# Optimization experiments

Measured on AMD Instinct MI355X. Metric: run time of the kernel, lower is better.

## Reference

```python
import jax, jax.numpy as jnp
import numpy as np

NUM_CLASS = 31
B = 4096
F_IN = 2048
F_BOT = 256


def setup_inputs() -> dict:
    key = jax.random.key(0)
    ks = jax.random.split(key, 6)
    return {
        "source": jax.random.normal(ks[0], (B, F_IN), dtype=jnp.float32),
        "target": jax.random.normal(ks[1], (B, F_IN), dtype=jnp.float32),
        "W_b": jax.random.normal(ks[2], (F_IN, F_BOT), dtype=jnp.float32) * (1.0 / np.sqrt(F_IN)),
        "b_b": jnp.zeros((F_BOT,), dtype=jnp.float32),
        "W_c": jax.random.normal(ks[3], (F_BOT, NUM_CLASS), dtype=jnp.float32) * (1.0 / np.sqrt(F_BOT)),
        "b_c": jnp.zeros((NUM_CLASS,), dtype=jnp.float32),
        "source_label": jax.random.randint(ks[4], (B,), 0, NUM_CLASS, dtype=jnp.int64),
    }


def _conf_margin(logits, labels):
    # get_confidence_output_margin: softmax confidence margin vs best wrong class
    conf = jax.nn.softmax(logits, axis=-1)
    mask = jax.nn.one_hot(labels, NUM_CLASS, dtype=conf.dtype)
    targets_conf = jnp.sum(conf * mask, axis=1)
    max_excl_conf = jnp.max(conf * (1.0 - mask), axis=1)
    return targets_conf - max_excl_conf


def _pairwise_sqdist(s, t):
    # ||x_p - x_q||^2 computed as a single GEMM + broadcast (replaces python double loop)
    s2 = jnp.sum(s * s, axis=1)  # [Bs]
    t2 = jnp.sum(t * t, axis=1)  # [Bt]
    d2 = s2[:, None] + t2[None, :] - 2.0 * (s @ t.T)
    return jnp.maximum(d2, 0.0)


def reference(source, target, W_b, b_b, W_c, b_c, source_label):
    # bottleneck: Linear + ReLU (shared weights for both domains)
    src = jax.nn.relu(source @ W_b + b_b)  # [B, 256]
    tar = jax.nn.relu(target @ W_b + b_b)  # [B, 256]

    src_clf = src @ W_c + b_c  # [B, 31]
    tar_clf = tar @ W_c + b_c  # [B, 31]

    # cross entropy on source
    logp = jax.nn.log_softmax(src_clf, axis=-1)
    clf_loss = -jnp.mean(jnp.take_along_axis(logp, source_label[:, None], axis=1))

    src_margin = _conf_margin(src_clf, source_label)
    tar_margin = _conf_margin(tar_clf, jnp.argmax(tar_clf, axis=1))

    # no_grad diagnostics: MMD + Gaussian kernel means (amplitude=1, sigma in {1,5})
    delta = jnp.mean(src, axis=0) - jnp.mean(tar, axis=0)
    curr_mmd = jax.lax.stop_gradient(delta @ delta)
    d2 = _pairwise_sqdist(src, tar)  # [B, B]
    curr_gk1 = jax.lax.stop_gradient(jnp.mean(jnp.exp(-0.5 * d2)))
    curr_gk5 = jax.lax.stop_gradient(jnp.mean(jnp.exp(-d2 / 50.0)))

    return jnp.concatenate([
        jnp.stack([clf_loss, curr_mmd, curr_gk1, curr_gk5]),
        src_margin,
        tar_margin,
    ])  # [4 + 2B]
```

## Files before the change

kernel.cpp:

```cpp
#include <hip/hip_runtime.h>
#include <stdint.h>

#define DI __device__ __forceinline__

typedef float f32x4 __attribute__((ext_vector_type(4)));
typedef short bf16x8 __attribute__((ext_vector_type(8)));

DI uint16_t f2bf(float f) {
    union { float f; uint32_t u; } v; v.f = f;
    uint32_t r = v.u + 0x7FFF + ((v.u >> 16) & 1);
    return (uint16_t)(r >> 16);
}
DI float bf2f(uint16_t h) {
    union { uint32_t u; float f; } v; v.u = ((uint32_t)h) << 16;
    return v.f;
}
DI void gl_lds16(const void* g, void* l) {
    __builtin_amdgcn_global_load_lds(
        (__attribute__((address_space(1))) void*)(uintptr_t)g,
        (__attribute__((address_space(3))) void*)(uintptr_t)l,
        16, 0, 0);
}

__global__ void k_init(const float* __restrict__ Wc, uint16_t* __restrict__ WcT,
                       float* __restrict__ accs) {
    int tid = threadIdx.x;
    if (tid < 4) accs[tid] = 0.f;
    for (int idx = tid; idx < 32 * 256; idx += 256) {
        int n = idx >> 8, k = idx & 255;
        WcT[idx] = (n < 31) ? f2bf(Wc[k * 31 + n]) : (uint16_t)0;
    }
}

__global__ void k_transpose_wb(const float* __restrict__ Wb, uint16_t* __restrict__ WbT) {
    __shared__ float t[32][33];
    int kb = blockIdx.x, nb = blockIdx.y;
    int tx = threadIdx.x & 31, ty0 = (threadIdx.x >> 5) * 4;
    for (int i = 0; i < 4; ++i)
        t[ty0 + i][tx] = Wb[(kb * 32 + ty0 + i) * 256 + nb * 32 + tx];
    __syncthreads();
    for (int i = 0; i < 4; ++i)
        WbT[(nb * 32 + ty0 + i) * 2048 + kb * 32 + tx] = f2bf(t[tx][ty0 + i]);
}

__launch_bounds__(256)
__global__ void k_bottleneck(const float* __restrict__ src, const float* __restrict__ tgt,
                             const uint16_t* __restrict__ WbT, const float* __restrict__ bb,
                             uint16_t* __restrict__ Y) {
    __shared__ __align__(16) uint8_t lds[32768];
    int tid = threadIdx.x;
    int lane = tid & 63, w = tid >> 6;
    int bm = blockIdx.x >> 2, bn = blockIdx.x & 3;
    int m0 = bm * 32;
    const float* X = (m0 < 4096) ? (src + (size_t)m0 * 2048)
                                 : (tgt + (size_t)(m0 - 4096) * 2048);
    int ar = tid >> 3, akb = (tid >> 2) & 1, ap = tid & 3;
    int ac = ap ^ (ar & 3) ^ ((ar >> 2) & 3);
    const float* Ag = X + ar * 2048 + akb * 32 + ac * 8;
    const int AwOff = akb * 2048 + ar * 64 + ap * 16;
    int cc = (lane >> 4) ^ (lane & 3) ^ ((lane >> 2) & 3);
    const uint16_t* Bg0; const uint16_t* Bg1;
    int lb0, lb1;
    {
        int p = lane & 3;
        #define BGADDR(ii) ({ int s_ = w * 2 + (ii); int kb_ = s_ >> 2; \
            int r_ = (s_ & 3) * 16 + (lane >> 2); \
            int c_ = p ^ (r_ & 3) ^ ((r_ >> 2) & 3); \
            WbT + (size_t)(bn * 64 + r_) * 2048 + kb_ * 32 + c_ * 8; })
        Bg0 = BGADDR(0); Bg1 = BGADDR(1);
        #undef BGADDR
        lb0 = (w * 2 + 0) * 1024;
        lb1 = (w * 2 + 1) * 1024;
    }
    int rnOff = (w * 16 + (lane & 15)) * 64 + cc * 16;

    f32x4 acc[2] = {};
    float4 rE0, rE1, rO0, rO1;

    #define STAGE_B(buf, k0) do { \
        gl_lds16(Bg0 + (k0), lds + 8192 + (buf) * 8192 + lb0); \
        gl_lds16(Bg1 + (k0), lds + 8192 + (buf) * 8192 + lb1); \
    } while (0)

    #define WRITE_A(par, r0v, r1v) do { \
        uint4 u_; \
        u_.x = (uint32_t)f2bf((r0v).x) | ((uint32_t)f2bf((r0v).y) << 16); \
        u_.y = (uint32_t)f2bf((r0v).z) | ((uint32_t)f2bf((r0v).w) << 16); \
        u_.z = (uint32_t)f2bf((r1v).x) | ((uint32_t)f2bf((r1v).y) << 16); \
        u_.w = (uint32_t)f2bf((r1v).z) | ((uint32_t)f2bf((r1v).w) << 16); \
        *(uint4*)(lds + (par) * 4096 + AwOff) = u_; \
    } while (0)

    #define COMPUTE(buf, par) do { \
        _Pragma("unroll") \
        for (int kb = 0; kb < 2; ++kb) { \
            bf16x8 a_[2], b_; \
            _Pragma("unroll") \
            for (int mi = 0; mi < 2; ++mi) \
                a_[mi] = *(const bf16x8*)(lds + (par) * 4096 + kb * 2048 + \
                                          (mi * 16 + (lane & 15)) * 64 + cc * 16); \
            b_ = *(const bf16x8*)(lds + 8192 + (buf) * 8192 + kb * 4096 + rnOff); \
            _Pragma("unroll") \
            for (int mi = 0; mi < 2; ++mi) \
                acc[mi] = __builtin_amdgcn_mfma_f32_16x16x32_bf16( \
                    a_[mi], b_, acc[mi], 0, 0, 0); \
        } \
    } while (0)

    #define FENCE() asm volatile("" ::: "memory")
    #define WAIT4() asm volatile("s_waitcnt vmcnt(4)" ::: "memory")
    #define WAIT0() asm volatile("s_waitcnt vmcnt(0)" ::: "memory")
    #define LGKM0_BAR() do { asm volatile("s_waitcnt lgkmcnt(0)" ::: "memory"); \
                             __builtin_amdgcn_s_barrier(); } while (0)

    STAGE_B(0, 0);
    FENCE();
    rE0 = *(const float4*)(Ag);
    rE1 = *(const float4*)(Ag + 4);
    FENCE();
    STAGE_B(1, 64);
    FENCE();
    rO0 = *(const float4*)(Ag + 64);
    rO1 = *(const float4*)(Ag + 68);
    WAIT4();
    WRITE_A(0, rE0, rE1);
    LGKM0_BAR();

    #define ITER(tc, BUF, NBUF, RL0, RL1, RW0, RW1, WPAR) do { \
        STAGE_B(NBUF, ((tc) + 2) * 64); \
        FENCE(); \
        RL0 = *(const float4*)(Ag + ((tc) + 2) * 64); \
        RL1 = *(const float4*)(Ag + ((tc) + 2) * 64 + 4); \
        FENCE(); \
        COMPUTE(BUF, (tc) & 1); \
        WAIT4();  \
        WRITE_A(WPAR, RW0, RW1); \
        LGKM0_BAR(); \
    } while (0)

    for (int t6 = 0; t6 < 5; ++t6) {
        int tb = t6 * 6;
        ITER(tb + 0, 0, 2, rE0, rE1, rO0, rO1, 1);
        ITER(tb + 1, 1, 0, rO0, rO1, rE0, rE1, 0);
        ITER(tb + 2, 2, 1, rE0, rE1, rO0, rO1, 1);
        ITER(tb + 3, 0, 2, rO0, rO1, rE0, rE1, 0);
        ITER(tb + 4, 1, 0, rE0, rE1, rO0, rO1, 1);
        ITER(tb + 5, 2, 1, rO0, rO1, rE0, rE1, 0);
    }
    COMPUTE(0, 0);
    WAIT0();
    WRITE_A(1, rO0, rO1);
    LGKM0_BAR();
    COMPUTE(1, 1);

    #undef ITER
    #undef STAGE_B
    #undef WRITE_A
    #undef COMPUTE
    #undef FENCE
    #undef WAIT4
    #undef WAIT0
    #undef LGKM0_BAR

    {
        int col = bn * 64 + w * 16 + (lane & 15);
        float bias = bb[col];
        for (int mi = 0; mi < 2; ++mi) {
            for (int j = 0; j < 4; ++j) {
                int row = m0 + mi * 16 + (lane >> 4) * 4 + j;
                float v = acc[mi][j] + bias;
                v = fmaxf(v, 0.f);
                Y[(size_t)row * 256 + col] = f2bf(v);
            }
        }
    }
}

__launch_bounds__(256)
__global__ void k_stats(const uint16_t* __restrict__ Y, float* __restrict__ s2t2,
                        float* __restrict__ colsum_part) {
    __shared__ float cs[4][256];
    int tid = threadIdx.x, lane = tid & 63, w = tid >> 6;
    int r0 = blockIdx.x * 32 + w * 8;
    float c0 = 0.f, c1 = 0.f, c2 = 0.f, c3 = 0.f;
    for (int i = 0; i < 8; ++i) {
        int row = r0 + i;
        ushort4 v = *(const ushort4*)(Y + (size_t)row * 256 + lane * 4);
        float a = bf2f(v.x), b = bf2f(v.y), c = bf2f(v.z), d = bf2f(v.w);
        c0 += a; c1 += b; c2 += c; c3 += d;
        float s = a * a + b * b + c * c + d * d;
        for (int m = 1; m < 64; m <<= 1) s += __shfl_xor(s, m);
        if (lane == 0) s2t2[row] = s;
    }
    cs[w][lane * 4 + 0] = c0;
    cs[w][lane * 4 + 1] = c1;
    cs[w][lane * 4 + 2] = c2;
    cs[w][lane * 4 + 3] = c3;
    __syncthreads();
    colsum_part[blockIdx.x * 256 + tid] =
        cs[0][tid] + cs[1][tid] + cs[2][tid] + cs[3][tid];
}

__launch_bounds__(256)
__global__ void k_classifier(const uint16_t* __restrict__ Y, const uint16_t* __restrict__ WcT,
                             const float* __restrict__ bc, const int* __restrict__ labels,
                             float* __restrict__ out_margin, float* __restrict__ ce_acc) {
    __shared__ __align__(16) uint8_t lds[49152];
    int tid = threadIdx.x, lane = tid & 63, w = tid >> 6;
    int m0 = blockIdx.x * 64;
    int cc = (lane >> 4) ^ (lane & 3) ^ ((lane >> 2) & 3);
    for (int s = w; s < 48; s += 4) {
        int r, p, c;
        if (s < 32) {
            int kb = s >> 2, r0 = (s & 3) * 16;
            r = r0 + (lane >> 2); p = lane & 3;
            c = p ^ (r & 3) ^ ((r >> 2) & 3);
            gl_lds16(Y + (size_t)(m0 + r) * 256 + kb * 32 + c * 8, lds + s * 1024);
        } else {
            int s2 = s - 32;
            int kb = s2 >> 1, r0 = (s2 & 1) * 16;
            r = r0 + (lane >> 2); p = lane & 3;
            c = p ^ (r & 3) ^ ((r >> 2) & 3);
            gl_lds16(WcT + r * 256 + kb * 32 + c * 8, lds + 32768 + s2 * 1024);
        }
    }
    __syncthreads();
    f32x4 acc[2] = {};
    for (int kb = 0; kb < 8; ++kb) {
        int r = w * 16 + (lane & 15);
        bf16x8 a = *(const bf16x8*)(lds + kb * 4096 + r * 64 + cc * 16);
        for (int nf = 0; nf < 2; ++nf) {
            int rn = nf * 16 + (lane & 15);
            bf16x8 b = *(const bf16x8*)(lds + 32768 + kb * 2048 + rn * 64 + cc * 16);
            acc[nf] = __builtin_amdgcn_mfma_f32_16x16x32_bf16(a, b, acc[nf], 0, 0, 0);
        }
    }
    int c0 = lane & 15, c1 = 16 + c0;
    float bc0 = bc[c0];
    float bc1 = (c1 < 31) ? bc[c1] : 0.f;
    bool is_src = (m0 < 4096);
    float ce_local = 0.f;
    for (int j = 0; j < 4; ++j) {
        int row = m0 + w * 16 + (lane >> 4) * 4 + j;
        float v0 = acc[0][j] + bc0;
        float v1 = (c1 < 31) ? (acc[1][j] + bc1) : -1e30f;
        float mx = fmaxf(v0, v1);
        for (int m = 1; m < 16; m <<= 1) mx = fmaxf(mx, __shfl_xor(mx, m, 16));
        float e0 = __expf(v0 - mx);
        float e1 = (c1 < 31) ? __expf(v1 - mx) : 0.f;
        float ssum = e0 + e1;
        for (int m = 1; m < 16; m <<= 1) ssum += __shfl_xor(ssum, m, 16);
        float inv = 1.f / ssum;
        float conf0 = e0 * inv, conf1 = e1 * inv;
        int lab;
        if (is_src) {
            lab = labels[row];
        } else {
            float bv; int bi;
            if (v0 >= v1) { bv = v0; bi = c0; } else { bv = v1; bi = c1; }
            for (int m = 1; m < 16; m <<= 1) {
                float ov = __shfl_xor(bv, m, 16);
                int oi = __shfl_xor(bi, m, 16);
                if (ov > bv || (ov == bv && oi < bi)) { bv = ov; bi = oi; }
            }
            lab = bi;
        }
        float tc = (c0 == lab ? conf0 : 0.f) + (c1 == lab ? conf1 : 0.f);
        for (int m = 1; m < 16; m <<= 1) tc += __shfl_xor(tc, m, 16);
        float ex = fmaxf(c0 == lab ? -1.f : conf0,
                         (c1 == lab || c1 >= 31) ? -1.f : conf1);
        for (int m = 1; m < 16; m <<= 1) ex = fmaxf(ex, __shfl_xor(ex, m, 16));
        if (c0 == 0) out_margin[row] = tc - ex;
        if (is_src) {
            float vl = (c0 == lab) ? v0 : ((c1 == lab) ? v1 : -1e30f);
            for (int m = 1; m < 16; m <<= 1) vl = fmaxf(vl, __shfl_xor(vl, m, 16));
            if (c0 == 0) ce_local += -(vl - mx - __logf(ssum));
        }
    }
    if (is_src) {
        ce_local += __shfl_xor(ce_local, 16);
        ce_local += __shfl_xor(ce_local, 32);
        if (lane == 0) atomicAdd(ce_acc, ce_local);
    }
}

__launch_bounds__(256)
__global__ void k_pairwise(const uint16_t* __restrict__ Y, const float* __restrict__ s2t2,
                           float* __restrict__ gk_part) {
    __shared__ __align__(16) uint8_t lds[65536];
    int tid = threadIdx.x, lane = tid & 63, w = tid >> 6;
    int m0 = blockIdx.x * 128, n0 = blockIdx.y * 128;
    int cc = (lane >> 4) ^ (lane & 3) ^ ((lane >> 2) & 3);
    int wm = (w & 1) * 64, wn = (w >> 1) * 64;
    f32x4 acc[4][4] = {};
    for (int h = 0; h < 2; ++h) {
        if (h) __syncthreads();
        int k0 = h * 128;
        for (int i = 0; i < 8; ++i) {
            int s = w * 8 + i;
            int kb = s >> 3, r0 = (s & 7) * 16;
            int r = r0 + (lane >> 2), p = lane & 3;
            int c = p ^ (r & 3) ^ ((r >> 2) & 3);
            gl_lds16(Y + (size_t)(m0 + r) * 256 + k0 + kb * 32 + c * 8, lds + s * 1024);
            gl_lds16(Y + (size_t)(4096 + n0 + r) * 256 + k0 + kb * 32 + c * 8,
                     lds + 32768 + s * 1024);
        }
        __syncthreads();
        for (int kb = 0; kb < 4; ++kb) {
            bf16x8 a[4], b[4];
            for (int mi = 0; mi < 4; ++mi) {
                int r = wm + mi * 16 + (lane & 15);
                a[mi] = *(const bf16x8*)(lds + kb * 8192 + r * 64 + cc * 16);
            }
            for (int nf = 0; nf < 4; ++nf) {
                int rn = wn + nf * 16 + (lane & 15);
                b[nf] = *(const bf16x8*)(lds + 32768 + kb * 8192 + rn * 64 + cc * 16);
            }
            for (int mi = 0; mi < 4; ++mi)
                for (int nf = 0; nf < 4; ++nf)
                    acc[mi][nf] = __builtin_amdgcn_mfma_f32_16x16x32_bf16(
                        a[mi], b[nf], acc[mi][nf], 0, 0, 0);
        }
    }
    float t2v[4];
    for (int nf = 0; nf < 4; ++nf)
        t2v[nf] = s2t2[4096 + n0 + wn + nf * 16 + (lane & 15)];
    float g1 = 0.f, g5 = 0.f;
    for (int mi = 0; mi < 4; ++mi) {
        int rbase = m0 + wm + mi * 16 + (lane >> 4) * 4;
        float s2v[4];
        for (int j = 0; j < 4; ++j) s2v[j] = s2t2[rbase + j];
        for (int nf = 0; nf < 4; ++nf)
            for (int j = 0; j < 4; ++j) {
                float d2 = s2v[j] + t2v[nf] - 2.f * acc[mi][nf][j];
                d2 = fmaxf(d2, 0.f);
                g1 += __expf(-0.5f * d2);
                g5 += __expf(-0.02f * d2);
            }
    }
    for (int m = 1; m < 64; m <<= 1) { g1 += __shfl_xor(g1, m); g5 += __shfl_xor(g5, m); }
    __syncthreads();
    float* red = (float*)lds;
    if (lane == 0) { red[w * 2] = g1; red[w * 2 + 1] = g5; }
    __syncthreads();
    if (tid == 0) {
        int bid = blockIdx.y * 32 + blockIdx.x;
        gk_part[bid * 2]     = red[0] + red[2] + red[4] + red[6];
        gk_part[bid * 2 + 1] = red[1] + red[3] + red[5] + red[7];
    }
}

__global__ void k_finalize(const float* __restrict__ colsum_part,
                           const float* __restrict__ gk_part,
                           const float* __restrict__ accs, float* __restrict__ d_out) {
    __shared__ float red[12];
    int tid = threadIdx.x, lane = tid & 63, w = tid >> 6;
    float cs = 0.f, ct = 0.f;
    for (int b = 0; b < 128; ++b)   cs += colsum_part[b * 256 + tid];
    for (int b = 128; b < 256; ++b) ct += colsum_part[b * 256 + tid];
    float delta = (cs - ct) * (1.f / 4096.f);
    float sq = delta * delta;
    float g1 = 0.f, g5 = 0.f;
    for (int i = 0; i < 4; ++i) {
        int p = tid * 4 + i;
        g1 += gk_part[p * 2];
        g5 += gk_part[p * 2 + 1];
    }
    for (int m = 1; m < 64; m <<= 1) {
        sq += __shfl_xor(sq, m);
        g1 += __shfl_xor(g1, m);
        g5 += __shfl_xor(g5, m);
    }
    if (lane == 0) { red[w * 3] = sq; red[w * 3 + 1] = g1; red[w * 3 + 2] = g5; }
    __syncthreads();
    if (tid == 0) {
        d_out[0] = accs[0] * (1.f / 4096.f);
        d_out[1] = red[0] + red[3] + red[6] + red[9];
        d_out[2] = (red[1] + red[4] + red[7] + red[10]) * 5.9604644775390625e-08f;
        d_out[3] = (red[2] + red[5] + red[8] + red[11]) * 5.9604644775390625e-08f;
    }
}

extern "C" void kernel_launch(void* const* d_in, const int* in_sizes, int n_in,
                              void* d_out, int out_size, void* d_ws, size_t ws_size,
                              hipStream_t stream) {
    const float* source = (const float*)d_in[0];
    const float* target = (const float*)d_in[1];
    const float* Wb     = (const float*)d_in[2];
    const float* bb     = (const float*)d_in[3];
    const float* Wc     = (const float*)d_in[4];
    const float* bc     = (const float*)d_in[5];
    const int*   labels = (const int*)d_in[6];
    float* out = (float*)d_out;
    uint8_t* ws = (uint8_t*)d_ws;

    uint16_t* Y    = (uint16_t*)(ws);
    uint16_t* WbT  = (uint16_t*)(ws + 4194304);
    uint16_t* WcT  = (uint16_t*)(ws + 5242880);
    float*    s2t2 = (float*)(ws + 5259264);
    float*    accs = (float*)(ws + 5292032);
    float*    colsum_part = (float*)(ws + 4194304);
    float*    gk_part     = (float*)(ws + 4194304 + 262144);

    k_init<<<1, 256, 0, stream>>>(Wc, WcT, accs);
    k_transpose_wb<<<dim3(64, 8), 256, 0, stream>>>(Wb, WbT);
    k_bottleneck<<<1024, 256, 0, stream>>>(source, target, WbT, bb, Y);
    k_stats<<<256, 256, 0, stream>>>(Y, s2t2, colsum_part);
    k_classifier<<<128, 256, 0, stream>>>(Y, WcT, bc, labels, out + 4, accs);
    k_pairwise<<<dim3(32, 32), 256, 0, stream>>>(Y, s2t2, gk_part);
    k_finalize<<<1, 256, 0, stream>>>(colsum_part, gk_part, accs, out);
}
```

Before: 184.2 us.

## Widen bottleneck GEMM tile to 128 columns to halve redundant A-tile loads

The bottleneck GEMM block now computes a 32x128 output tile instead of 32x64, so each block stages four B chunks per k-step and each wave issues four MFMAs per k-slice over two N fragments. The grid shrinks from 1024 to 512 blocks, so each fp32 input row block is loaded and converted to bf16 twice instead of four times. LDS grows to 56 KB per block and accumulator registers double, which may lower occupancy, and fewer blocks give less parallelism across CUs.

```diff
diff --git a/kernel.cpp b/kernel.cpp
--- a/kernel.cpp
+++ b/kernel.cpp
@@ -47,10 +47,10 @@
 __global__ void k_bottleneck(const float* __restrict__ src, const float* __restrict__ tgt,
                              const uint16_t* __restrict__ WbT, const float* __restrict__ bb,
                              uint16_t* __restrict__ Y) {
-    __shared__ __align__(16) uint8_t lds[32768];
+    __shared__ __align__(16) uint8_t lds[57344];
     int tid = threadIdx.x;
     int lane = tid & 63, w = tid >> 6;
-    int bm = blockIdx.x >> 2, bn = blockIdx.x & 3;
+    int bm = blockIdx.x >> 1, bn = blockIdx.x & 1;
     int m0 = bm * 32;
     const float* X = (m0 < 4096) ? (src + (size_t)m0 * 2048)
                                  : (tgt + (size_t)(m0 - 4096) * 2048);
@@ -59,27 +59,27 @@
     const float* Ag = X + ar * 2048 + akb * 32 + ac * 8;
     const int AwOff = akb * 2048 + ar * 64 + ap * 16;
     int cc = (lane >> 4) ^ (lane & 3) ^ ((lane >> 2) & 3);
-    const uint16_t* Bg0; const uint16_t* Bg1;
-    int lb0, lb1;
+    const uint16_t* Bg0; const uint16_t* Bg1; const uint16_t* Bg2; const uint16_t* Bg3;
     {
         int p = lane & 3;
-        #define BGADDR(ii) ({ int s_ = w * 2 + (ii); int kb_ = s_ >> 2; \
-            int r_ = (s_ & 3) * 16 + (lane >> 2); \
+        int i0 = w * 4;
+        #define BGADDR(ii) ({ int s_ = i0 + (ii); int kb_ = s_ >> 3; \
+            int r_ = (s_ & 7) * 16 + (lane >> 2); \
             int c_ = p ^ (r_ & 3) ^ ((r_ >> 2) & 3); \
-            WbT + (size_t)(bn * 64 + r_) * 2048 + kb_ * 32 + c_ * 8; })
-        Bg0 = BGADDR(0); Bg1 = BGADDR(1);
+            WbT + (size_t)(bn * 128 + r_) * 2048 + kb_ * 32 + c_ * 8; })
+        Bg0 = BGADDR(0); Bg1 = BGADDR(1); Bg2 = BGADDR(2); Bg3 = BGADDR(3);
         #undef BGADDR
-        lb0 = (w * 2 + 0) * 1024;
-        lb1 = (w * 2 + 1) * 1024;
-    }
-    int rnOff = (w * 16 + (lane & 15)) * 64 + cc * 16;
-
-    f32x4 acc[2] = {};
+    }
+    const int lbB = 8192 + w * 4096;
+
+    f32x4 acc[2][2] = {};
     float4 rE0, rE1, rO0, rO1;
 
     #define STAGE_B(buf, k0) do { \
-        gl_lds16(Bg0 + (k0), lds + 8192 + (buf) * 8192 + lb0); \
-        gl_lds16(Bg1 + (k0), lds + 8192 + (buf) * 8192 + lb1); \
+        gl_lds16(Bg0 + (k0), lds + lbB + (buf) * 16384 + 0);    \
+        gl_lds16(Bg1 + (k0), lds + lbB + (buf) * 16384 + 1024); \
+        gl_lds16(Bg2 + (k0), lds + lbB + (buf) * 16384 + 2048); \
+        gl_lds16(Bg3 + (k0), lds + lbB + (buf) * 16384 + 3072); \
     } while (0)
 
     #define WRITE_A(par, r0v, r1v) do { \
@@ -94,21 +94,26 @@
     #define COMPUTE(buf, par) do { \
         _Pragma("unroll") \
         for (int kb = 0; kb < 2; ++kb) { \
-            bf16x8 a_[2], b_; \
+            bf16x8 a_[2], b_[2]; \
             _Pragma("unroll") \
             for (int mi = 0; mi < 2; ++mi) \
                 a_[mi] = *(const bf16x8*)(lds + (par) * 4096 + kb * 2048 + \
                                           (mi * 16 + (lane & 15)) * 64 + cc * 16); \
-            b_ = *(const bf16x8*)(lds + 8192 + (buf) * 8192 + kb * 4096 + rnOff); \
+            _Pragma("unroll") \
+            for (int nf = 0; nf < 2; ++nf) \
+                b_[nf] = *(const bf16x8*)(lds + 8192 + (buf) * 16384 + kb * 8192 + \
+                                          (w * 32 + nf * 16 + (lane & 15)) * 64 + cc * 16); \
             _Pragma("unroll") \
             for (int mi = 0; mi < 2; ++mi) \
-                acc[mi] = __builtin_amdgcn_mfma_f32_16x16x32_bf16( \
-                    a_[mi], b_, acc[mi], 0, 0, 0); \
+                _Pragma("unroll") \
+                for (int nf = 0; nf < 2; ++nf) \
+                    acc[mi][nf] = __builtin_amdgcn_mfma_f32_16x16x32_bf16( \
+                        a_[mi], b_[nf], acc[mi][nf], 0, 0, 0); \
         } \
     } while (0)
 
     #define FENCE() asm volatile("" ::: "memory")
-    #define WAIT4() asm volatile("s_waitcnt vmcnt(4)" ::: "memory")
+    #define WAIT6() asm volatile("s_waitcnt vmcnt(6)" ::: "memory")
     #define WAIT0() asm volatile("s_waitcnt vmcnt(0)" ::: "memory")
     #define LGKM0_BAR() do { asm volatile("s_waitcnt lgkmcnt(0)" ::: "memory"); \
                              __builtin_amdgcn_s_barrier(); } while (0)
@@ -122,18 +127,18 @@
     FENCE();
     rO0 = *(const float4*)(Ag + 64);
     rO1 = *(const float4*)(Ag + 68);
-    WAIT4();
+    WAIT6();
     WRITE_A(0, rE0, rE1);
     LGKM0_BAR();
 
     #define ITER(tc, BUF, NBUF, RL0, RL1, RW0, RW1, WPAR) do { \
-        STAGE_B(NBUF, ((tc) + 2) * 64); \
+        STAGE_B(NBUF, ((tc) + 2) * 64);   \
         FENCE(); \
         RL0 = *(const float4*)(Ag + ((tc) + 2) * 64); \
         RL1 = *(const float4*)(Ag + ((tc) + 2) * 64 + 4); \
         FENCE(); \
         COMPUTE(BUF, (tc) & 1); \
-        WAIT4();  \
+        WAIT6();  \
         WRITE_A(WPAR, RW0, RW1); \
         LGKM0_BAR(); \
     } while (0)
@@ -158,22 +163,21 @@
     #undef WRITE_A
     #undef COMPUTE
     #undef FENCE
-    #undef WAIT4
+    #undef WAIT6
     #undef WAIT0
     #undef LGKM0_BAR
 
-    {
-        int col = bn * 64 + w * 16 + (lane & 15);
-        float bias = bb[col];
-        for (int mi = 0; mi < 2; ++mi) {
+    for (int mi = 0; mi < 2; ++mi)
+        for (int nf = 0; nf < 2; ++nf) {
+            int col = bn * 128 + w * 32 + nf * 16 + (lane & 15);
+            float bias = bb[col];
             for (int j = 0; j < 4; ++j) {
                 int row = m0 + mi * 16 + (lane >> 4) * 4 + j;
-                float v = acc[mi][j] + bias;
+                float v = acc[mi][nf][j] + bias;
                 v = fmaxf(v, 0.f);
                 Y[(size_t)row * 256 + col] = f2bf(v);
             }
         }
-    }
 }
 
 __launch_bounds__(256)
@@ -404,7 +408,7 @@
 
     k_init<<<1, 256, 0, stream>>>(Wc, WcT, accs);
     k_transpose_wb<<<dim3(64, 8), 256, 0, stream>>>(Wb, WbT);
-    k_bottleneck<<<1024, 256, 0, stream>>>(source, target, WbT, bb, Y);
+    k_bottleneck<<<512, 256, 0, stream>>>(source, target, WbT, bb, Y);
     k_stats<<<256, 256, 0, stream>>>(Y, s2t2, colsum_part);
     k_classifier<<<128, 256, 0, stream>>>(Y, WcT, bc, labels, out + 4, accs);
     k_pairwise<<<dim3(32, 32), 256, 0, stream>>>(Y, s2t2, gk_part);
```

Result: faster. 175.7 us (-4.6%).
